# Kernel tuning notes

Measured on AMD Instinct MI355X. Metric: run time of the kernel, lower is better.

## Reference

```python
import jax, jax.numpy as jnp
import numpy as np

B, IN_CH, OUT_CH, N_GRID, MODES = 64, 64, 64, 2048, 512


def _dct1_matrix(N, dtype=jnp.float32):
    """Matrix M s.t. (x @ M.T) == scipy.fftpack.dct(x, type=1, axis=-1).
    DCT-I: y[k] = x[0] + (-1)^k x[N-1] + 2*sum_{n=1}^{N-2} x[n] cos(pi k n/(N-1)).
    Note scipy's unnormalized idct(type=1) is the same transform, so M also
    implements chebyshev_inverse."""
    k = jnp.arange(N, dtype=jnp.float32)
    M = jnp.cos(jnp.pi * jnp.outer(k, k) / (N - 1))
    c = jnp.full((N,), 2.0, dtype=jnp.float32).at[0].set(1.0).at[N - 1].set(1.0)
    return (M * c[None, :]).astype(dtype)


def setup_inputs() -> dict:
    key = jax.random.key(0)
    kx, kw = jax.random.split(key)
    x = jax.random.normal(kx, (B, IN_CH, N_GRID), dtype=jnp.float32)
    # xavier_uniform on (in, out, modes): fan_in=in, fan_out=out (per torch for 3D params)
    bound = float(np.sqrt(6.0 / (IN_CH + OUT_CH)))
    weights = jax.random.uniform(kw, (IN_CH, OUT_CH, MODES), minval=-bound,
                                 maxval=bound, dtype=jnp.float32)
    return {"x": x, "weights": weights}


def reference(x, weights):
    # x: [b, in, n]; weights: [in, out, modes]
    N = x.shape[-1]
    modes = weights.shape[-1]
    M = _dct1_matrix(N, x.dtype)
    # forward Chebyshev (DCT-I) transform along grid axis
    x_cheb = jnp.einsum('bin,kn->bik', x, M)          # [b, in, n]
    # mix modes: keep first `modes` coefficients, zero the rest
    out_modes = jnp.einsum('bix,iox->box', x_cheb[..., :modes], weights)
    out_cheb = jnp.pad(out_modes, ((0, 0), (0, 0), (0, N - modes)))
    # inverse transform (scipy unnormalized IDCT-I == DCT-I)
    return jnp.einsum('bok,nk->bon', out_cheb, M)     # [b, out, n]
```

## Files before the change

kernel.cpp:

```cpp
#include <hip/hip_runtime.h>

typedef unsigned short u16;
typedef __attribute__((ext_vector_type(8))) short short8;
typedef __attribute__((ext_vector_type(4))) float f32x4;

#define B_  64
#define IC  64
#define OC  64
#define NG  2048
#define MD  512

__device__ inline u16 f2b(float f) {
  unsigned u = __float_as_uint(f);
  unsigned r = (u + 0x7FFFu + ((u >> 16) & 1u)) >> 16;
  return (u16)r;
}

__device__ __forceinline__ void gld_lds16(const u16* g, const u16* l) {
  __builtin_amdgcn_global_load_lds(
      (__attribute__((address_space(1))) void*)(uintptr_t)(g),
      (__attribute__((address_space(3))) void*)(unsigned)(uintptr_t)(l),
      16, 0, 0);
}

__global__ __launch_bounds__(256) void prep(
    const float* __restrict__ x, const float* __restrict__ w,
    u16* __restrict__ xb, u16* __restrict__ wT2,
    u16* __restrict__ M1, u16* __restrict__ M3) {
  __shared__ float S[64][65];
  const int id = blockIdx.x;
  const int t = threadIdx.x;
  if (id < 8192) {
    int i = (id * 256 + t) * 4;
    float4 v = *(const float4*)(x + i);
    ushort4 o;
    o.x = f2b(v.x); o.y = f2b(v.y); o.z = f2b(v.z); o.w = f2b(v.w);
    *(ushort4*)(xb + i) = o;
  } else if (id < 8704) {
    int wb = id - 8192;
    int o = wb & 63, kb = wb >> 6;
    int r0 = t >> 6, c = t & 63;
#pragma unroll
    for (int j = 0; j < 16; ++j) {
      int i = r0 + j * 4;
      S[i][c] = w[(size_t)(i * 64 + o) * MD + kb * 64 + c];
    }
    __syncthreads();
#pragma unroll
    for (int j = 0; j < 16; ++j) {
      int kk = r0 + j * 4;
      wT2[(size_t)(kb * 64 + kk) * 4096 + o * 64 + c] = f2b(S[c][kk]);
    }
  } else if (id < 12800) {
    int idx = (id - 8704) * 256 + t;
    int k = idx >> 11, n = idx & 2047;
    int r = (k * n) % (2 * (NG - 1));
    float ang = (float)r * (3.14159265358979323846f / (NG - 1));
    float v = __cosf(ang) * ((n == 0 || n == NG - 1) ? 1.0f : 2.0f);
    M1[idx] = f2b(v);
  } else {
    int idx = (id - 12800) * 256 + t;
    int n = idx >> 9, k = idx & 511;
    int r = (n * k) % (2 * (NG - 1));
    float ang = (float)r * (3.14159265358979323846f / (NG - 1));
    float v = __cosf(ang) * ((k == 0) ? 1.0f : 2.0f);
    M3[idx] = f2b(v);
  }
}

template<int MI, int NI, bool OUT_BF16>
__global__ __launch_bounds__(256, 2) void gemm_bt3(
    const u16* __restrict__ A,
    const u16* __restrict__ Bt,
    void* __restrict__ Cv,
    int K, int N) {
  constexpr int TM = MI * 32;
  constexpr int TN = NI * 32;
  constexpr int BK = 64;
  constexpr int ROWS = TM + TN;
  constexpr int CH = ROWS / 4;
  constexpr int NISSUE = CH / 8;
  constexpr int BUF = ROWS * BK;
  __shared__ u16 S[2 * BUF];

  const int tid  = threadIdx.x;
  const int lane = tid & 63;
  const int wave = tid >> 6;
  const int wm = (wave >> 1) * (MI * 16);
  const int wn = (wave & 1) * (NI * 16);
  const long bm = (long)blockIdx.y * TM;
  const long bn = (long)blockIdx.x * TN;

  const int lrow = lane & 15;
  const int lhi  = lane >> 4;

  const int scc = (((lane & 7) ^ (lane >> 3)) * 8);
  const int r0 = wave * CH;

  const u16* gsrc[NISSUE];
  unsigned lofs[NISSUE];
#pragma unroll
  for (int ii = 0; ii < NISSUE; ++ii) {
    int rr = r0 + ii * 8 + (lane >> 3);
    gsrc[ii] = (rr < TM) ? (A + (bm + rr) * (long)K + scc)
                         : (Bt + (bn + rr - TM) * (long)K + scc);
    lofs[ii] = (unsigned)((r0 + ii * 8) * BK);
  }

  f32x4 acc[MI][NI] = {};

#pragma unroll
  for (int ii = 0; ii < NISSUE; ++ii)
    gld_lds16(gsrc[ii], &S[lofs[ii]]);

  int p = 0;
  for (int k0 = 0; k0 < K; k0 += BK) {
    __syncthreads();

    if (k0 + BK < K) {
#pragma unroll
      for (int ii = 0; ii < NISSUE; ++ii)
        gld_lds16(gsrc[ii] + k0 + BK, &S[(1 - p) * BUF + lofs[ii]]);
    }

    const u16* Sp = &S[p * BUF];
#pragma unroll
    for (int kk8 = 0; kk8 < 8; kk8 += 4) {
      short8 af[MI], bfr[NI];
#pragma unroll
      for (int i = 0; i < MI; ++i) {
        int pch = ((kk8 + lhi) ^ (lane & 7));
        af[i] = *(const short8*)&Sp[(wm + i * 16 + lrow) * BK + pch * 8];
      }
#pragma unroll
      for (int j = 0; j < NI; ++j) {
        int pch = ((kk8 + lhi) ^ (lane & 7));
        bfr[j] = *(const short8*)&Sp[(TM + wn + j * 16 + lrow) * BK + pch * 8];
      }
#pragma unroll
      for (int i = 0; i < MI; ++i)
#pragma unroll
        for (int j = 0; j < NI; ++j)
          acc[i][j] = __builtin_amdgcn_mfma_f32_16x16x32_bf16(af[i], bfr[j], acc[i][j], 0, 0, 0);
    }
    p ^= 1;
  }

  const int crow = (lane >> 4) * 4;
  const int ccol = lane & 15;
#pragma unroll
  for (int i = 0; i < MI; ++i)
#pragma unroll
    for (int j = 0; j < NI; ++j) {
      long gm = bm + wm + i * 16 + crow;
      long gn = bn + wn + j * 16 + ccol;
      if (OUT_BF16) {
        u16* cp = (u16*)Cv + gm * (long)N + gn;
#pragma unroll
        for (int r = 0; r < 4; ++r)
          cp[(long)r * N] = f2b(acc[i][j][r]);
      } else {
        float* cp = (float*)Cv + gm * (long)N + gn;
#pragma unroll
        for (int r = 0; r < 4; ++r)
          cp[(long)r * N] = acc[i][j][r];
      }
    }
}

__global__ __launch_bounds__(256, 4) void mode_mix_mfma(
    const u16* __restrict__ xcT,
    const u16* __restrict__ wT2,
    u16* __restrict__ omT) {
  constexpr int PK = 72;
  __shared__ u16 S[128 * PK];
  const int k = blockIdx.x;
  const int t = threadIdx.x;

#pragma unroll
  for (int c = 0; c < 4; ++c) {
    int ch = t + c * 256;
    int half = ch >> 9, cc = ch & 511;
    int row = cc >> 3, col8 = cc & 7;
    const u16* src = half ? wT2 : xcT;
    uint4 v = *(const uint4*)(src + (size_t)k * 4096 + row * 64 + col8 * 8);
    *(uint4*)&S[(half * 64 + row) * PK + col8 * 8] = v;
  }
  __syncthreads();

  const int lane = t & 63;
  const int wave = t >> 6;
  const int wm = (wave >> 1) * 32;
  const int wn = (wave & 1) * 32;
  const int lrow = lane & 15;
  const int lhi  = lane >> 4;

  f32x4 acc[2][2] = {};
#pragma unroll
  for (int kk8 = 0; kk8 < 8; kk8 += 4) {
    short8 af[2], bfr[2];
#pragma unroll
    for (int i = 0; i < 2; ++i)
      af[i] = *(const short8*)&S[(wm + i * 16 + lrow) * PK + (kk8 + lhi) * 8];
#pragma unroll
    for (int j = 0; j < 2; ++j)
      bfr[j] = *(const short8*)&S[(64 + wn + j * 16 + lrow) * PK + (kk8 + lhi) * 8];
#pragma unroll
    for (int i = 0; i < 2; ++i)
#pragma unroll
      for (int j = 0; j < 2; ++j)
        acc[i][j] = __builtin_amdgcn_mfma_f32_16x16x32_bf16(af[i], bfr[j], acc[i][j], 0, 0, 0);
  }

  const int crow = (lane >> 4) * 4;
  const int ccol = lane & 15;
#pragma unroll
  for (int i = 0; i < 2; ++i)
#pragma unroll
    for (int j = 0; j < 2; ++j) {
      int b = wm + i * 16 + crow;
      int o = wn + j * 16 + ccol;
#pragma unroll
      for (int r = 0; r < 4; ++r)
        omT[(size_t)k * 4096 + (b + r) * 64 + o] = f2b(acc[i][j][r]);
    }
}

__global__ __launch_bounds__(256) void transpose_om(const u16* __restrict__ omT,
                                                    u16* __restrict__ om) {
  __shared__ u16 S[64][65];
  const int bb = blockIdx.x;
  const int kb = blockIdx.y;
  const int t = threadIdx.x;
  const int r0 = t >> 6;
  const int c  = t & 63;
#pragma unroll
  for (int j = 0; j < 16; ++j) {
    int kr = r0 + j * 4;
    S[kr][c] = omT[(size_t)(kb * 64 + kr) * 4096 + bb * 64 + c];
  }
  __syncthreads();
#pragma unroll
  for (int j = 0; j < 16; ++j) {
    int br = r0 + j * 4;
    om[(size_t)(bb * 64 + br) * MD + kb * 64 + c] = S[c][br];
  }
}

extern "C" void kernel_launch(void* const* d_in, const int* in_sizes, int n_in,
                              void* d_out, int out_size, void* d_ws, size_t ws_size,
                              hipStream_t stream) {
  const float* x = (const float*)d_in[0];
  const float* w = (const float*)d_in[1];
  float* out = (float*)d_out;

  char* ws = (char*)d_ws;
  u16* xb  = (u16*)ws;
  u16* M1  = (u16*)(ws + (size_t)16 * 1024 * 1024);
  u16* M3  = (u16*)(ws + (size_t)18 * 1024 * 1024);
  u16* xcT = (u16*)(ws + (size_t)20 * 1024 * 1024);
  u16* wT2 = (u16*)(ws + (size_t)24 * 1024 * 1024);
  u16* omT = (u16*)(ws + (size_t)28 * 1024 * 1024);
  u16* om  = (u16*)(ws + (size_t)32 * 1024 * 1024);

  prep<<<16896, 256, 0, stream>>>(x, w, xb, wT2, M1, M3);

  gemm_bt3<2, 2, true><<<dim3((B_ * IC) / 64, MD / 64), 256, 0, stream>>>(
      M1, xb, xcT, NG, B_ * IC);

  mode_mix_mfma<<<MD, 256, 0, stream>>>(xcT, wT2, omT);

  transpose_om<<<dim3((B_ * OC) / 64, MD / 64), 256, 0, stream>>>(omT, om);

  gemm_bt3<4, 4, false><<<dim3(NG / 128, (B_ * OC) / 128), 256, 0, stream>>>(
      om, M3, out, MD, NG);
}
```

Baseline: 129.8 us.

## Exploit DCT-I even/odd symmetry to halve both transform GEMMs

```diff
diff --git a/kernel.cpp b/kernel.cpp
--- a/kernel.cpp
+++ b/kernel.cpp
@@ -16,6 +16,11 @@
   return (u16)r;
 }
 
+__device__ __forceinline__ float cosk(int k, int n) {
+  int r = (k * n) % (2 * (NG - 1));
+  return __cosf((float)r * (3.14159265358979323846f / (NG - 1)));
+}
+
 __device__ __forceinline__ void gld_lds16(const u16* g, const u16* l) {
   __builtin_amdgcn_global_load_lds(
       (__attribute__((address_space(1))) void*)(uintptr_t)(g),
@@ -25,53 +30,64 @@
 
 __global__ __launch_bounds__(256) void prep(
     const float* __restrict__ x, const float* __restrict__ w,
-    u16* __restrict__ xb, u16* __restrict__ wT2,
-    u16* __restrict__ M1, u16* __restrict__ M3) {
+    u16* __restrict__ e, u16* __restrict__ o, u16* __restrict__ wT2,
+    u16* __restrict__ M1p, u16* __restrict__ M3e, u16* __restrict__ M3o) {
   __shared__ float S[64][65];
   const int id = blockIdx.x;
   const int t = threadIdx.x;
-  if (id < 8192) {
-    int i = (id * 256 + t) * 4;
-    float4 v = *(const float4*)(x + i);
-    ushort4 o;
-    o.x = f2b(v.x); o.y = f2b(v.y); o.z = f2b(v.z); o.w = f2b(v.w);
-    *(ushort4*)(xb + i) = o;
-  } else if (id < 8704) {
-    int wb = id - 8192;
-    int o = wb & 63, kb = wb >> 6;
+  if (id < 4096) {
+    const float* xr = x + (size_t)id * NG;
+    float4 f = *(const float4*)(xr + 4 * t);
+    float4 b = *(const float4*)(xr + (2044 - 4 * t));
+    ushort4 ev, ov;
+    ev.x = f2b(f.x + b.w); ov.x = f2b(f.x - b.w);
+    ev.y = f2b(f.y + b.z); ov.y = f2b(f.y - b.z);
+    ev.z = f2b(f.z + b.y); ov.z = f2b(f.z - b.y);
+    ev.w = f2b(f.w + b.x); ov.w = f2b(f.w - b.x);
+    *(ushort4*)(e + (size_t)id * 1024 + 4 * t) = ev;
+    *(ushort4*)(o + (size_t)id * 1024 + 4 * t) = ov;
+  } else if (id < 4608) {
+    int wb = id - 4096;
+    int oo = wb & 63, kb = wb >> 6;
     int r0 = t >> 6, c = t & 63;
 #pragma unroll
     for (int j = 0; j < 16; ++j) {
       int i = r0 + j * 4;
-      S[i][c] = w[(size_t)(i * 64 + o) * MD + kb * 64 + c];
+      S[i][c] = w[(size_t)(i * 64 + oo) * MD + kb * 64 + c];
     }
     __syncthreads();
 #pragma unroll
     for (int j = 0; j < 16; ++j) {
       int kk = r0 + j * 4;
-      wT2[(size_t)(kb * 64 + kk) * 4096 + o * 64 + c] = f2b(S[c][kk]);
-    }
-  } else if (id < 12800) {
-    int idx = (id - 8704) * 256 + t;
-    int k = idx >> 11, n = idx & 2047;
-    int r = (k * n) % (2 * (NG - 1));
-    float ang = (float)r * (3.14159265358979323846f / (NG - 1));
-    float v = __cosf(ang) * ((n == 0 || n == NG - 1) ? 1.0f : 2.0f);
-    M1[idx] = f2b(v);
+      wT2[(size_t)(kb * 64 + kk) * 4096 + oo * 64 + c] = f2b(S[c][kk]);
+    }
+  } else if (id < 6656) {
+    int idx = (id - 4608) * 256 + t;
+    int r = idx >> 10, n = idx & 1023;
+    int k = (r < 256) ? 2 * r : 2 * (r - 256) + 1;
+    float v = cosk(k, n) * ((n == 0) ? 1.0f : 2.0f);
+    M1p[idx] = f2b(v);
   } else {
-    int idx = (id - 12800) * 256 + t;
-    int n = idx >> 9, k = idx & 511;
-    int r = (n * k) % (2 * (NG - 1));
-    float ang = (float)r * (3.14159265358979323846f / (NG - 1));
-    float v = __cosf(ang) * ((k == 0) ? 1.0f : 2.0f);
-    M3[idx] = f2b(v);
+    int idx = (id - 6656) * 256 + t;
+    int half = idx >> 18;
+    int rem = idx & 262143;
+    int n = rem >> 8, kp = rem & 255;
+    if (half == 0) {
+      float v = cosk(2 * kp, n) * ((kp == 0) ? 1.0f : 2.0f);
+      M3e[rem] = f2b(v);
+    } else {
+      float v = cosk(2 * kp + 1, n) * 2.0f;
+      M3o[rem] = f2b(v);
+    }
   }
 }
 
 template<int MI, int NI, bool OUT_BF16>
 __global__ __launch_bounds__(256, 2) void gemm_bt3(
     const u16* __restrict__ A,
-    const u16* __restrict__ Bt,
+    const u16* __restrict__ Bt0,
+    const u16* __restrict__ Bt1,
+    int splitY,
     void* __restrict__ Cv,
     int K, int N) {
   constexpr int TM = MI * 32;
@@ -90,6 +106,7 @@
   const int wn = (wave & 1) * (NI * 16);
   const long bm = (long)blockIdx.y * TM;
   const long bn = (long)blockIdx.x * TN;
+  const u16* Bt = ((int)blockIdx.y < splitY) ? Bt0 : Bt1;
 
   const int lrow = lane & 15;
   const int lhi  = lane >> 4;
@@ -175,6 +192,7 @@
   constexpr int PK = 72;
   __shared__ u16 S[128 * PK];
   const int k = blockIdx.x;
+  const int rk = (k & 1) ? 256 + (k >> 1) : (k >> 1);
   const int t = threadIdx.x;
 
 #pragma unroll
@@ -182,8 +200,9 @@
     int ch = t + c * 256;
     int half = ch >> 9, cc = ch & 511;
     int row = cc >> 3, col8 = cc & 7;
-    const u16* src = half ? wT2 : xcT;
-    uint4 v = *(const uint4*)(src + (size_t)k * 4096 + row * 64 + col8 * 8);
+    const u16* src = half ? (wT2 + (size_t)k * 4096)
+                          : (xcT + (size_t)rk * 4096);
+    uint4 v = *(const uint4*)(src + row * 64 + col8 * 8);
     *(uint4*)&S[(half * 64 + row) * PK + col8 * 8] = v;
   }
   __syncthreads();
@@ -219,15 +238,15 @@
 #pragma unroll
     for (int j = 0; j < 2; ++j) {
       int b = wm + i * 16 + crow;
-      int o = wn + j * 16 + ccol;
+      int oo = wn + j * 16 + ccol;
 #pragma unroll
       for (int r = 0; r < 4; ++r)
-        omT[(size_t)k * 4096 + (b + r) * 64 + o] = f2b(acc[i][j][r]);
+        omT[(size_t)k * 4096 + (b + r) * 64 + oo] = f2b(acc[i][j][r]);
     }
 }
 
 __global__ __launch_bounds__(256) void transpose_om(const u16* __restrict__ omT,
-                                                    u16* __restrict__ om) {
+                                                    u16* __restrict__ omp) {
   __shared__ u16 S[64][65];
   const int bb = blockIdx.x;
   const int kb = blockIdx.y;
@@ -240,11 +259,100 @@
     S[kr][c] = omT[(size_t)(kb * 64 + kr) * 4096 + bb * 64 + c];
   }
   __syncthreads();
+  const int col = ((c & 1) ? 256 : 0) + kb * 32 + (c >> 1);
 #pragma unroll
   for (int j = 0; j < 16; ++j) {
     int br = r0 + j * 4;
-    om[(size_t)(bb * 64 + br) * MD + kb * 64 + c] = S[c][br];
-  }
+    omp[(size_t)(bb * 64 + br) * MD + col] = S[c][br];
+  }
+}
+
+__global__ __launch_bounds__(256, 2) void gemm_g3(
+    const u16* __restrict__ omp,
+    const u16* __restrict__ M3e,
+    const u16* __restrict__ M3o,
+    float* __restrict__ out) {
+  constexpr int BK = 64;
+  constexpr int ROWS = 384;
+  constexpr int CH = ROWS / 4;
+  constexpr int NISSUE = CH / 8;
+  __shared__ u16 S[ROWS * BK];
+
+  const int tid  = threadIdx.x;
+  const int lane = tid & 63;
+  const int wave = tid >> 6;
+  const long bm = (long)blockIdx.y * 128;
+  const int n0 = blockIdx.x * 64;
+
+  const int lrow = lane & 15;
+  const int lhi  = lane >> 4;
+  const int scc = (((lane & 7) ^ (lane >> 3)) * 8);
+  const int r0 = wave * CH;
+
+  const u16* gsrc[NISSUE];
+  unsigned lofs[NISSUE];
+#pragma unroll
+  for (int ii = 0; ii < NISSUE; ++ii) {
+    int rr = r0 + ii * 8 + (lane >> 3);
+    const u16* p;
+    if (rr < 128)       p = omp + (bm + rr) * (long)512 + scc;
+    else if (rr < 256)  p = omp + (bm + rr - 128) * (long)512 + 256 + scc;
+    else if (rr < 320)  p = M3e + (n0 + rr - 256) * (long)256 + scc;
+    else                p = M3o + (n0 + rr - 320) * (long)256 + scc;
+    gsrc[ii] = p;
+    lofs[ii] = (unsigned)((r0 + ii * 8) * BK);
+  }
+
+  f32x4 accE[2][4] = {};
+  f32x4 accO[2][4] = {};
+
+  for (int k0 = 0; k0 < 256; k0 += BK) {
+#pragma unroll
+    for (int ii = 0; ii < NISSUE; ++ii)
+      gld_lds16(gsrc[ii] + k0, &S[lofs[ii]]);
+    __syncthreads();
+
+#pragma unroll
+    for (int kk8 = 0; kk8 < 8; kk8 += 4) {
+      int pch = ((kk8 + lhi) ^ (lane & 7));
+      short8 aE[2], aO[2], bE[4], bO[4];
+#pragma unroll
+      for (int i = 0; i < 2; ++i) {
+        aE[i] = *(const short8*)&S[(wave * 32 + i * 16 + lrow) * BK + pch * 8];
+        aO[i] = *(const short8*)&S[(128 + wave * 32 + i * 16 + lrow) * BK + pch * 8];
+      }
+#pragma unroll
+      for (int j = 0; j < 4; ++j) {
+        bE[j] = *(const short8*)&S[(256 + j * 16 + lrow) * BK + pch * 8];
+        bO[j] = *(const short8*)&S[(320 + j * 16 + lrow) * BK + pch * 8];
+      }
+#pragma unroll
+      for (int i = 0; i < 2; ++i)
+#pragma unroll
+        for (int j = 0; j < 4; ++j) {
+          accE[i][j] = __builtin_amdgcn_mfma_f32_16x16x32_bf16(aE[i], bE[j], accE[i][j], 0, 0, 0);
+          accO[i][j] = __builtin_amdgcn_mfma_f32_16x16x32_bf16(aO[i], bO[j], accO[i][j], 0, 0, 0);
+        }
+    }
+    __syncthreads();
+  }
+
+  const int crow = (lane >> 4) * 4;
+  const int ccol = lane & 15;
+#pragma unroll
+  for (int i = 0; i < 2; ++i)
+#pragma unroll
+    for (int j = 0; j < 4; ++j) {
+      long bo = bm + wave * 32 + i * 16 + crow;
+      int n = n0 + j * 16 + ccol;
+      float* op = out + bo * (long)NG;
+#pragma unroll
+      for (int r = 0; r < 4; ++r) {
+        float E = accE[i][j][r], O = accO[i][j][r];
+        op[(long)r * NG + n] = E + O;
+        op[(long)r * NG + (NG - 1 - n)] = E - O;
+      }
+    }
 }
 
 extern "C" void kernel_launch(void* const* d_in, const int* in_sizes, int n_in,
@@ -255,23 +363,24 @@
   float* out = (float*)d_out;
 
   char* ws = (char*)d_ws;
-  u16* xb  = (u16*)ws;
-  u16* M1  = (u16*)(ws + (size_t)16 * 1024 * 1024);
-  u16* M3  = (u16*)(ws + (size_t)18 * 1024 * 1024);
-  u16* xcT = (u16*)(ws + (size_t)20 * 1024 * 1024);
-  u16* wT2 = (u16*)(ws + (size_t)24 * 1024 * 1024);
-  u16* omT = (u16*)(ws + (size_t)28 * 1024 * 1024);
-  u16* om  = (u16*)(ws + (size_t)32 * 1024 * 1024);
-
-  prep<<<16896, 256, 0, stream>>>(x, w, xb, wT2, M1, M3);
-
-  gemm_bt3<2, 2, true><<<dim3((B_ * IC) / 64, MD / 64), 256, 0, stream>>>(
-      M1, xb, xcT, NG, B_ * IC);
+  u16* e    = (u16*)ws;
+  u16* o    = (u16*)(ws + (size_t)8 * 1024 * 1024);
+  u16* M1p  = (u16*)(ws + (size_t)16 * 1024 * 1024);
+  u16* M3e  = (u16*)(ws + (size_t)17 * 1024 * 1024);
+  u16* M3o  = (u16*)(ws + (size_t)17 * 1024 * 1024 + 512 * 1024);
+  u16* xcT  = (u16*)(ws + (size_t)20 * 1024 * 1024);
+  u16* wT2  = (u16*)(ws + (size_t)24 * 1024 * 1024);
+  u16* omT  = (u16*)(ws + (size_t)28 * 1024 * 1024);
+  u16* omp  = (u16*)(ws + (size_t)32 * 1024 * 1024);
+
+  prep<<<8704, 256, 0, stream>>>(x, w, e, o, wT2, M1p, M3e, M3o);
+
+  gemm_bt3<2, 2, true><<<dim3((B_ * IC) / 64, 512 / 64), 256, 0, stream>>>(
+      M1p, e, o, 4, xcT, 1024, B_ * IC);
 
   mode_mix_mfma<<<MD, 256, 0, stream>>>(xcT, wT2, omT);
 
-  transpose_om<<<dim3((B_ * OC) / 64, MD / 64), 256, 0, stream>>>(omT, om);
-
-  gemm_bt3<4, 4, false><<<dim3(NG / 128, (B_ * OC) / 128), 256, 0, stream>>>(
-      om, M3, out, MD, NG);
-}
+  transpose_om<<<dim3((B_ * OC) / 64, MD / 64), 256, 0, stream>>>(omT, omp);
+
+  gemm_g3<<<dim3(1024 / 64, (B_ * OC) / 128), 256, 0, stream>>>(omp, M3e, M3o, out);
+}
```

Measured after the change: 118.0 us. 9.1% less time.
